# Performance work log

Hardware: AMD Instinct MI355X
Metric: run time of the kernel (lower is better)

The kernel has to match this reference:

```python
import jax, jax.numpy as jnp
import numpy as np

N = 500_000   # nodes
D = 128       # feature dim (init arg d)
B = 1024      # number of graphs / segments
EPS = 1e-6


def setup_inputs() -> dict:
    key = jax.random.key(0)
    k_x, k_b, k_ps, k_qs, k_w, k_bias = jax.random.split(key, 6)
    x = jax.random.normal(k_x, (N, D), dtype=jnp.float32)
    batch = jnp.sort(jax.random.randint(k_b, (N,), 0, B)).astype(jnp.int64)
    ps_raw = jax.random.normal(k_ps, (2,), dtype=jnp.float32)
    qs_raw = jax.random.normal(k_qs, (2,), dtype=jnp.float32)
    W = jax.random.normal(k_w, (D, D), dtype=jnp.float32) / np.sqrt(D)
    b = jax.random.normal(k_bias, (D,), dtype=jnp.float32) * 0.01
    return {"x": x, "batch": batch, "ps_raw": ps_raw, "qs_raw": qs_raw, "W": W, "b": b}


def reference(x, batch, ps_raw, qs_raw, W, b):
    # ps = -Threshold(thr=-50, val=50)(-softplus(ps_raw))
    sp = jax.nn.softplus(ps_raw)
    ps = -jnp.where(-sp > -50.0, -sp, 50.0)
    qs = jnp.tanh(qs_raw)

    # per-graph node counts: global_add_pool(ones)
    nums = jax.ops.segment_sum(jnp.ones(x.shape[0], dtype=x.dtype), batch,
                               num_segments=B)[:, None]            # (B, 1)

    xa = jnp.abs(x) + EPS                                           # (N, D)
    d1 = xa.shape[1] // 2                                           # split feature dim

    # positive branch: exp(p0 * log(x)) == x**p0, summed per graph
    x_pos = jnp.exp(ps[0] * jnp.log(xa[:, :d1]))                    # (N, d1)
    s_pos = jax.ops.segment_sum(x_pos, batch, num_segments=B)       # (B, d1)
    gnp_pos = jnp.exp(jnp.log(s_pos) / ps[0]) / nums ** qs[0]

    # negative branch: plain power / root p-norm form
    s_neg = jax.ops.segment_sum(xa[:, d1:] ** ps[1], batch, num_segments=B)  # (B, D-d1)
    gnp_neg = s_neg ** (1.0 / ps[1]) / nums ** qs[0]

    gnp = jnp.concatenate([gnp_pos, gnp_neg], axis=1)               # (B, D)
    return gnp @ W.T + b
```

## Files before the change

### kernel.cpp

```cpp
#include <hip/hip_runtime.h>
#include <math.h>

#define NSEG   1024
#define DFEAT  128
#define EPS_F  1e-6f
#define NCHUNK 8192

__device__ __forceinline__ float softplus_thr(float v) {
    float sp = log1pf(__expf(v));
    return (sp >= 50.0f) ? -50.0f : sp;
}

__global__ __launch_bounds__(64)
void segsum_kernel(const float* __restrict__ x,
                   const int*   __restrict__ batch,
                   const float* __restrict__ ps_raw,
                   float* __restrict__ s,
                   float* __restrict__ cnt,
                   int n_nodes, int chunk)
{
    const int t = threadIdx.x;
    const int start = blockIdx.x * chunk;
    if (start >= n_nodes) return;
    const int end = min(start + chunk, n_nodes);

    const float p = softplus_thr(ps_raw[(t < 32) ? 0 : 1]);

    const float2* __restrict__ x2 = (const float2*)x;

    int   cur = batch[start];
    float accx = 0.0f, accy = 0.0f;
    int   run = 0;

    for (int n = start; n < end; ++n) {
        const int sg = batch[n];
        if (sg != cur) {
            atomicAdd(&s[(size_t)cur * DFEAT + 2 * t],     accx);
            atomicAdd(&s[(size_t)cur * DFEAT + 2 * t + 1], accy);
            if (t == 0) atomicAdd(&cnt[cur], (float)run);
            accx = 0.0f; accy = 0.0f; run = 0; cur = sg;
        }
        const float2 v = x2[(size_t)n * 64 + t];
        const float ax = fabsf(v.x) + EPS_F;
        const float ay = fabsf(v.y) + EPS_F;
        accx += __expf(p * __logf(ax));
        accy += __expf(p * __logf(ay));
        ++run;
    }
    atomicAdd(&s[(size_t)cur * DFEAT + 2 * t],     accx);
    atomicAdd(&s[(size_t)cur * DFEAT + 2 * t + 1], accy);
    if (t == 0) atomicAdd(&cnt[cur], (float)run);
}

__global__ __launch_bounds__(128)
void finalize_gemm_kernel(const float* __restrict__ s,
                          const float* __restrict__ cnt,
                          const float* __restrict__ ps_raw,
                          const float* __restrict__ qs_raw,
                          const float* __restrict__ W,
                          const float* __restrict__ bias,
                          float* __restrict__ out)
{
    __shared__ float g[DFEAT];
    const int b = blockIdx.x;
    const int i = threadIdx.x;

    const float p  = softplus_thr(ps_raw[(i < 64) ? 0 : 1]);
    const float q0 = tanhf(qs_raw[0]);

    const float n     = cnt[b];
    const float scale = __expf(-q0 * __logf(n));
    const float sv    = s[(size_t)b * DFEAT + i];
    g[i] = __expf(__logf(sv) / p) * scale;
    __syncthreads();

    const float4* __restrict__ W4 = (const float4*)(W + (size_t)i * DFEAT);
    float acc = bias[i];
#pragma unroll
    for (int jj = 0; jj < DFEAT / 4; ++jj) {
        const float4 w = W4[jj];
        acc += g[4 * jj]     * w.x;
        acc += g[4 * jj + 1] * w.y;
        acc += g[4 * jj + 2] * w.z;
        acc += g[4 * jj + 3] * w.w;
    }
    out[(size_t)b * DFEAT + i] = acc;
}

extern "C" void kernel_launch(void* const* d_in, const int* in_sizes, int n_in,
                              void* d_out, int out_size, void* d_ws, size_t ws_size,
                              hipStream_t stream)
{
    const float* x      = (const float*)d_in[0];
    const int*   batch  = (const int*)  d_in[1];
    const float* ps_raw = (const float*)d_in[2];
    const float* qs_raw = (const float*)d_in[3];
    const float* W      = (const float*)d_in[4];
    const float* bias   = (const float*)d_in[5];
    float*       out    = (float*)d_out;

    const int n_nodes = in_sizes[0] / DFEAT;

    float* s   = (float*)d_ws;
    float* cnt = s + (size_t)NSEG * DFEAT;

    hipMemsetAsync(d_ws, 0, sizeof(float) * ((size_t)NSEG * DFEAT + NSEG), stream);

    const int chunk = (n_nodes + NCHUNK - 1) / NCHUNK;
    segsum_kernel<<<NCHUNK, 64, 0, stream>>>(x, batch, ps_raw, s, cnt, n_nodes, chunk);
    finalize_gemm_kernel<<<NSEG, 128, 0, stream>>>(s, cnt, ps_raw, qs_raw, W, bias, out);
}
```

Baseline: 373.4 us.

## Fuse segment pooling and GEMM into one per-segment kernel via binary search

Replaces the chunked atomic segment-sum kernel, the memset and the separate finalize/GEMM kernel with a single kernel that gives each segment one 512-thread block. Each block binary-searches the sorted batch array for its bounds, reduces rows with float4 loads across 16 row-slots, combines the partials in shared memory, and then applies the power-mean normalization and the W projection. This removes global atomics, the workspace memset and one launch. In exchange only 1024 blocks are launched, so load balance depends on how evenly nodes are spread over segments, and each block pays for two binary searches.

Result: no change. 370.3 us (-0.8%).

```diff
diff --git a/kernel.cpp b/kernel.cpp
--- a/kernel.cpp
+++ b/kernel.cpp
@@ -4,87 +4,77 @@
 #define NSEG   1024
 #define DFEAT  128
 #define EPS_F  1e-6f
-#define NCHUNK 8192
 
 __device__ __forceinline__ float softplus_thr(float v) {
     float sp = log1pf(__expf(v));
     return (sp >= 50.0f) ? -50.0f : sp;
 }
 
-__global__ __launch_bounds__(64)
-void segsum_kernel(const float* __restrict__ x,
-                   const int*   __restrict__ batch,
-                   const float* __restrict__ ps_raw,
-                   float* __restrict__ s,
-                   float* __restrict__ cnt,
-                   int n_nodes, int chunk)
+__global__ __launch_bounds__(512, 8)
+void fused_pool_kernel(const float* __restrict__ x,
+                       const int*   __restrict__ batch,
+                       const float* __restrict__ ps_raw,
+                       const float* __restrict__ qs_raw,
+                       const float* __restrict__ W,
+                       const float* __restrict__ bias,
+                       float* __restrict__ out,
+                       int n_nodes)
 {
-    const int t = threadIdx.x;
-    const int start = blockIdx.x * chunk;
-    if (start >= n_nodes) return;
-    const int end = min(start + chunk, n_nodes);
+    const int b    = blockIdx.x;
+    const int tid  = threadIdx.x;
+    const int w    = tid >> 6;
+    const int lane = tid & 63;
+    const int half = lane >> 5;
+    const int f4   = lane & 31;
 
-    const float p = softplus_thr(ps_raw[(t < 32) ? 0 : 1]);
+    int lo0 = 0, hi0 = n_nodes;
+    int lo1 = 0, hi1 = n_nodes;
+    while (lo0 < hi0) { int m = (lo0 + hi0) >> 1; if (batch[m] < b)     lo0 = m + 1; else hi0 = m; }
+    while (lo1 < hi1) { int m = (lo1 + hi1) >> 1; if (batch[m] < b + 1) lo1 = m + 1; else hi1 = m; }
+    const int start = lo0, end = lo1;
 
-    const float2* __restrict__ x2 = (const float2*)x;
+    const float p = softplus_thr(ps_raw[(f4 < 16) ? 0 : 1]);
 
-    int   cur = batch[start];
-    float accx = 0.0f, accy = 0.0f;
-    int   run = 0;
+    const float4* __restrict__ x4 = (const float4*)x;
+    float a0 = 0.f, a1 = 0.f, a2 = 0.f, a3 = 0.f;
+#pragma unroll 2
+    for (int r = start + 2 * w + half; r < end; r += 16) {
+        const float4 v = x4[(size_t)r * 32 + f4];
+        a0 += __expf(p * __logf(fabsf(v.x) + EPS_F));
+        a1 += __expf(p * __logf(fabsf(v.y) + EPS_F));
+        a2 += __expf(p * __logf(fabsf(v.z) + EPS_F));
+        a3 += __expf(p * __logf(fabsf(v.w) + EPS_F));
+    }
 
-    for (int n = start; n < end; ++n) {
-        const int sg = batch[n];
-        if (sg != cur) {
-            atomicAdd(&s[(size_t)cur * DFEAT + 2 * t],     accx);
-            atomicAdd(&s[(size_t)cur * DFEAT + 2 * t + 1], accy);
-            if (t == 0) atomicAdd(&cnt[cur], (float)run);
-            accx = 0.0f; accy = 0.0f; run = 0; cur = sg;
-        }
-        const float2 v = x2[(size_t)n * 64 + t];
-        const float ax = fabsf(v.x) + EPS_F;
-        const float ay = fabsf(v.y) + EPS_F;
-        accx += __expf(p * __logf(ax));
-        accy += __expf(p * __logf(ay));
-        ++run;
-    }
-    atomicAdd(&s[(size_t)cur * DFEAT + 2 * t],     accx);
-    atomicAdd(&s[(size_t)cur * DFEAT + 2 * t + 1], accy);
-    if (t == 0) atomicAdd(&cnt[cur], (float)run);
-}
-
-__global__ __launch_bounds__(128)
-void finalize_gemm_kernel(const float* __restrict__ s,
-                          const float* __restrict__ cnt,
-                          const float* __restrict__ ps_raw,
-                          const float* __restrict__ qs_raw,
-                          const float* __restrict__ W,
-                          const float* __restrict__ bias,
-                          float* __restrict__ out)
-{
+    __shared__ float part[16][DFEAT + 4];
     __shared__ float g[DFEAT];
-    const int b = blockIdx.x;
-    const int i = threadIdx.x;
-
-    const float p  = softplus_thr(ps_raw[(i < 64) ? 0 : 1]);
-    const float q0 = tanhf(qs_raw[0]);
-
-    const float n     = cnt[b];
-    const float scale = __expf(-q0 * __logf(n));
-    const float sv    = s[(size_t)b * DFEAT + i];
-    g[i] = __expf(__logf(sv) / p) * scale;
+    float4* dst = (float4*)&part[2 * w + half][4 * f4];
+    *dst = make_float4(a0, a1, a2, a3);
     __syncthreads();
 
-    const float4* __restrict__ W4 = (const float4*)(W + (size_t)i * DFEAT);
-    float acc = bias[i];
+    if (tid < DFEAT) {
+        float ssum = 0.f;
+#pragma unroll
+        for (int k = 0; k < 16; ++k) ssum += part[k][tid];
+        const float pf = softplus_thr(ps_raw[(tid < 64) ? 0 : 1]);
+        const float q0 = tanhf(qs_raw[0]);
+        const float n  = (float)(end - start);
+        g[tid] = __expf(__logf(ssum) / pf - q0 * __logf(n));
+    }
+    __syncthreads();
+
+    if (tid >= DFEAT) return;
+
+    const float4* __restrict__ W4 = (const float4*)(W + (size_t)tid * DFEAT);
+    const float4* g4 = (const float4*)g;
+    float acc = bias[tid];
 #pragma unroll
     for (int jj = 0; jj < DFEAT / 4; ++jj) {
-        const float4 w = W4[jj];
-        acc += g[4 * jj]     * w.x;
-        acc += g[4 * jj + 1] * w.y;
-        acc += g[4 * jj + 2] * w.z;
-        acc += g[4 * jj + 3] * w.w;
+        const float4 wv = W4[jj];
+        const float4 gv = g4[jj];
+        acc += gv.x * wv.x + gv.y * wv.y + gv.z * wv.z + gv.w * wv.w;
     }
-    out[(size_t)b * DFEAT + i] = acc;
+    out[(size_t)b * DFEAT + tid] = acc;
 }
 
 extern "C" void kernel_launch(void* const* d_in, const int* in_sizes, int n_in,
@@ -101,12 +91,6 @@
 
     const int n_nodes = in_sizes[0] / DFEAT;
 
-    float* s   = (float*)d_ws;
-    float* cnt = s + (size_t)NSEG * DFEAT;
-
-    hipMemsetAsync(d_ws, 0, sizeof(float) * ((size_t)NSEG * DFEAT + NSEG), stream);
-
-    const int chunk = (n_nodes + NCHUNK - 1) / NCHUNK;
-    segsum_kernel<<<NCHUNK, 64, 0, stream>>>(x, batch, ps_raw, s, cnt, n_nodes, chunk);
-    finalize_gemm_kernel<<<NSEG, 128, 0, stream>>>(s, cnt, ps_raw, qs_raw, W, bias, out);
+    fused_pool_kernel<<<NSEG, 512, 0, stream>>>(x, batch, ps_raw, qs_raw,
+                                                W, bias, out, n_nodes);
 }
```
